# Kernel tuning notes

Measured on AMD Instinct MI355X. Metric: run time of the kernel, lower is better.

Reference implementation:

```python
import jax, jax.numpy as jnp
import numpy as np

B, T, H, L = 32, 512, 1024, 3


def setup_inputs() -> dict:
    key = jax.random.key(0)
    k1, k2, k3, k4 = jax.random.split(key, 4)
    scale = H ** -0.5  # stand-in for orthogonal init scale
    x = jax.random.normal(k1, (B, T, H), dtype=jnp.float32)
    h_0 = jax.random.normal(k2, (L, B, H), dtype=jnp.float32)
    w_ih = jax.random.normal(k3, (L, 3 * H, H), dtype=jnp.float32) * scale
    w_hh = jax.random.normal(k4, (L, 3 * H, H), dtype=jnp.float32) * scale
    b_ih = jnp.zeros((L, 3 * H), dtype=jnp.float32)  # module zero-inits biases
    b_hh = jnp.zeros((L, 3 * H), dtype=jnp.float32)
    return {"x": x, "h_0": h_0, "w_ih": w_ih, "w_hh": w_hh, "b_ih": b_ih, "b_hh": b_hh}


def _gru_layer(x_seq, h0, w_ih, w_hh, b_ih, b_hh):
    # Precompute input-side gate projections for all timesteps in one GEMM.
    gi = jnp.einsum('bti,gi->btg', x_seq, w_ih) + b_ih  # [B,T,3H]
    gi = jnp.transpose(gi, (1, 0, 2))  # [T,B,3H]

    def step(h, gi_t):
        gh = h @ w_hh.T + b_hh  # [B,3H]
        i_r, i_z, i_n = jnp.split(gi_t, 3, axis=-1)
        h_r, h_z, h_n = jnp.split(gh, 3, axis=-1)
        r = jax.nn.sigmoid(i_r + h_r)
        z = jax.nn.sigmoid(i_z + h_z)
        n = jnp.tanh(i_n + r * h_n)
        h_new = (1.0 - z) * n + z * h
        return h_new, h_new

    h_last, out = jax.lax.scan(step, h0, gi)  # out: [T,B,H]
    return jnp.transpose(out, (1, 0, 2)), h_last


def reference(x, h_0, w_ih, w_hh, b_ih, b_hh):
    # Multi-layer batch_first GRU, dropout=0 (inference-equivalent).
    h_n = []
    seq = x
    for l in range(L):
        seq, h_last = _gru_layer(seq, h_0[l], w_ih[l], w_hh[l], b_ih[l], b_hh[l])
        h_n.append(h_last)
    return seq, jnp.stack(h_n, axis=0)  # out:[B,T,H], h_n:[L,B,H]
```

## Files before the change

### kernel.cpp

```cpp
#include <hip/hip_runtime.h>
#include <hip/hip_bf16.h>
#include <stdint.h>

#define HD   1024
#define BB   32
#define TT   512
#define LL   3
#define H3   3072
#define MTOT (BB*TT)

#define PLSZ 32768
#define WSL2 12288

typedef unsigned short u16;
typedef short bf16x8 __attribute__((ext_vector_type(8)));
typedef float f32x4 __attribute__((ext_vector_type(4)));

__device__ __forceinline__ u16 f2bf_bits(float f) {
    __hip_bfloat16 h = __float2bfloat16(f);
    return __builtin_bit_cast(u16, h);
}
__device__ __forceinline__ float bf_bits2f(u16 b) {
    return __bfloat162float(__builtin_bit_cast(__hip_bfloat16, b));
}

__device__ __forceinline__ void split8(const f32x4 v0, const f32x4 v1,
                                       bf16x8& hi, bf16x8& lo) {
#pragma unroll
    for (int e = 0; e < 4; ++e) {
        u16 h = f2bf_bits(v0[e]);
        hi[e] = (short)h;
        lo[e] = (short)f2bf_bits(v0[e] - bf_bits2f(h));
        u16 h2 = f2bf_bits(v1[e]);
        hi[4 + e] = (short)h2;
        lo[4 + e] = (short)f2bf_bits(v1[e] - bf_bits2f(h2));
    }
}

__global__ void split_f32_kernel(const float* __restrict__ in,
                                 u16* __restrict__ hi, u16* __restrict__ lo, int n4) {
    int i = blockIdx.x * blockDim.x + threadIdx.x;
    int stride = gridDim.x * blockDim.x;
    for (; i < n4; i += stride) {
        float4 v = ((const float4*)in)[i];
        ushort4 h, l;
        float f;
        f = v.x; h.x = f2bf_bits(f); l.x = f2bf_bits(f - bf_bits2f(h.x));
        f = v.y; h.y = f2bf_bits(f); l.y = f2bf_bits(f - bf_bits2f(h.y));
        f = v.z; h.z = f2bf_bits(f); l.z = f2bf_bits(f - bf_bits2f(h.z));
        f = v.w; h.w = f2bf_bits(f); l.w = f2bf_bits(f - bf_bits2f(h.w));
        ((ushort4*)hi)[i] = h;
        ((ushort4*)lo)[i] = l;
    }
}

__global__ void tobf_kernel(const float* __restrict__ in, u16* __restrict__ out, int n4) {
    int i = blockIdx.x * blockDim.x + threadIdx.x;
    int stride = gridDim.x * blockDim.x;
    for (; i < n4; i += stride) {
        float4 v = ((const float4*)in)[i];
        ushort4 h;
        h.x = f2bf_bits(v.x); h.y = f2bf_bits(v.y);
        h.z = f2bf_bits(v.z); h.w = f2bf_bits(v.w);
        ((ushort4*)out)[i] = h;
    }
}

__global__ __launch_bounds__(256) void pack_w_kernel(
    const float* __restrict__ whh, const float* __restrict__ wih,
    u16* __restrict__ wslab, u16* __restrict__ wislab)
{
    const int l  = blockIdx.x >> 8;
    const int ug = blockIdx.x & 255;
    const int n0 = ug * 4;
    const int tid = threadIdx.x;
    const int j = tid >> 4, c16 = tid & 15;
    if (j >= 12) return;
    const size_t rowoff = ((size_t)(j >> 2) * HD + n0 + (j & 3)) * HD;
    const float* wh = whh + (size_t)l * H3 * HD;
    const float* wi = wih + (size_t)l * H3 * HD;
    u16* dh = wslab + ((size_t)l * 256 + ug) * WSL2;
    u16* di = (l > 0) ? (wislab + ((size_t)(l - 1) * 256 + ug) * WSL2) : (u16*)nullptr;
#pragma unroll
    for (int c = 0; c < 8; ++c) {
        int kc = c16 + c * 16;
        f32x4 v0 = *(const f32x4*)(wh + rowoff + kc * 8);
        f32x4 v1 = *(const f32x4*)(wh + rowoff + kc * 8 + 4);
        bf16x8 hi, lo;
        split8(v0, v1, hi, lo);
        *(bf16x8*)(dh + (kc * 12 + j) * 8) = hi;
        if (l > 0) {
            f32x4 u0 = *(const f32x4*)(wi + rowoff + kc * 8);
            f32x4 u1 = *(const f32x4*)(wi + rowoff + kc * 8 + 4);
            bf16x8 ihi, dum;
            split8(u0, u1, ihi, dum);
            *(bf16x8*)(di + (kc * 12 + j) * 8) = ihi;
        }
    }
}

__global__ void pack_h0_kernel(const float* __restrict__ h0,
                               float* __restrict__ hb, u16* __restrict__ ht) {
    int idx = blockIdx.x * 256 + threadIdx.x;
    int l = idx >> 15;
    int rem = idx & 32767;
    int b = rem >> 10, n = rem & 1023;
    float f = h0[idx];
    hb[(size_t)(l * 2) * BB * HD + rem] = f;
    u16 hbits = f2bf_bits(f);
    u16 lbits = f2bf_bits(f - bf_bits2f(hbits));
    size_t o = ((size_t)(l * 2) * 2) * PLSZ + ((size_t)(n >> 3) * 32 + b) * 8 + (n & 7);
    ht[o] = hbits;
    ht[o + PLSZ] = lbits;
}

#define BM 128
#define BN 128
#define BK 32
#define LDSROW 40

__global__ __launch_bounds__(256) void gemm2p_kernel(
    const u16* __restrict__ Ahi, const u16* __restrict__ Alo,
    const u16* __restrict__ Wn,
    const float* __restrict__ bias,
    u16* __restrict__ Cout)
{
    __shared__ u16 sAh[BM * LDSROW];
    __shared__ u16 sAl[BM * LDSROW];
    __shared__ u16 sB [BN * LDSROW];

    const int tid  = threadIdx.x;
    const int lane = tid & 63;
    const int w    = tid >> 6;
    const int wr   = w >> 1, wc = w & 1;
    const int fr   = lane & 15;
    const int kg   = lane >> 4;

    const int bm = blockIdx.x & 127;
    const int bn = blockIdx.x >> 7;
    const int bmBase = bm * BM;
    const int bnBase = bn * BN;

    f32x4 acc[4][4] = {};

    for (int kt = 0; kt < 1024; kt += BK) {
        uint4 ra[2], rl[2], rb[2];
#pragma unroll
        for (int it = 0; it < 2; ++it) {
            int c = it * 256 + tid;
            int row = c >> 2, seg = c & 3;
            size_t ga = (size_t)(bmBase + row) * 1024 + kt + seg * 8;
            ra[it] = *(const uint4*)(Ahi + ga);
            rl[it] = *(const uint4*)(Alo + ga);
            size_t gb = (size_t)(bnBase + row) * 1024 + kt + seg * 8;
            rb[it] = *(const uint4*)(Wn + gb);
        }
        __syncthreads();
#pragma unroll
        for (int it = 0; it < 2; ++it) {
            int c = it * 256 + tid;
            int row = c >> 2, seg = c & 3;
            int lo = row * LDSROW + seg * 8;
            *(uint4*)(sAh + lo) = ra[it];
            *(uint4*)(sAl + lo) = rl[it];
            *(uint4*)(sB  + lo) = rb[it];
        }
        __syncthreads();

        bf16x8 fah[4], fal[4], fb[4];
#pragma unroll
        for (int mi = 0; mi < 4; ++mi) {
            int r = wr * 64 + mi * 16 + fr;
            fah[mi] = *(const bf16x8*)(sAh + r * LDSROW + kg * 8);
            fal[mi] = *(const bf16x8*)(sAl + r * LDSROW + kg * 8);
        }
#pragma unroll
        for (int ni = 0; ni < 4; ++ni) {
            int r = wc * 64 + ni * 16 + fr;
            fb[ni] = *(const bf16x8*)(sB + r * LDSROW + kg * 8);
        }
#pragma unroll
        for (int mi = 0; mi < 4; ++mi)
#pragma unroll
            for (int ni = 0; ni < 4; ++ni) {
                acc[mi][ni] = __builtin_amdgcn_mfma_f32_16x16x32_bf16(fah[mi], fb[ni], acc[mi][ni], 0, 0, 0);
                acc[mi][ni] = __builtin_amdgcn_mfma_f32_16x16x32_bf16(fal[mi], fb[ni], acc[mi][ni], 0, 0, 0);
            }
    }

#pragma unroll
    for (int mi = 0; mi < 4; ++mi)
#pragma unroll
        for (int ni = 0; ni < 4; ++ni) {
            int n = bnBase + wc * 64 + ni * 16 + fr;
            float bv = bias[n];
#pragma unroll
            for (int r = 0; r < 4; ++r) {
                int m = bmBase + wr * 64 + mi * 16 + kg * 4 + r;
                int b_ = m >> 9, t_ = m & 511;
                Cout[(size_t)(t_ * BB + b_) * H3 + n] = f2bf_bits(acc[mi][ni][r] + bv);
            }
        }
}

#define SGRID 768

__global__ __launch_bounds__(256) void gru_step_kernel(
    const u16* __restrict__ wslab,
    const u16* __restrict__ wislab,
    const float* __restrict__ bih, const float* __restrict__ bhh,
    const u16* __restrict__ gi0,
    float* __restrict__ hb,
    u16* __restrict__ ht,
    float* __restrict__ seqout, float* __restrict__ hnout, int k)
{
    const int layer = blockIdx.x >> 8;
    const int t = k - layer;
    if (t < 0 || t >= TT) return;
    const int ug = blockIdx.x & 255;
    const int n0 = ug * 4;
    const int tid = threadIdx.x, lane = tid & 63, w = tid >> 6;
    const int arow = lane & 15, akg = lane >> 4;

    __shared__ float Cp[4][2][2][16][16];

    const int xl = (layer > 0) ? layer - 1 : 0;
    const u16* hsH = ht + ((size_t)(layer * 2 + (t & 1)) * 2) * PLSZ;
    const u16* hsL = hsH + PLSZ;
    const u16* xsH = ht + ((size_t)(xl * 2 + ((t + 1) & 1)) * 2) * PLSZ;
    const u16* xsL = xsH + PLSZ;
    const u16* whH = wslab + ((size_t)layer * 256 + ug) * WSL2;
    const u16* wiH = wislab + ((size_t)xl * 256 + ug) * WSL2;

    float gi_0 = 0.f, gi_1 = 0.f, gi_2 = 0.f;
    if (layer == 0 && tid < 128) {
        const u16* gp = gi0 + (size_t)(t * BB + (tid >> 2)) * H3 + n0 + (tid & 3);
        gi_0 = bf_bits2f(gp[0]);
        gi_1 = bf_bits2f(gp[HD]);
        gi_2 = bf_bits2f(gp[2 * HD]);
    }

    f32x4 agh[2] = {};
    f32x4 agx[2] = {};

#pragma unroll
    for (int kt = 0; kt < 8; ++kt) {
        const int kc = w * 32 + kt * 4 + akg;
        const int aoff = (kc * 32 + arow) * 8;
        bf16x8 a0h = *(const bf16x8*)(hsH + aoff);
        bf16x8 a0l = *(const bf16x8*)(hsL + aoff);
        bf16x8 a1h = *(const bf16x8*)(hsH + aoff + 128);
        bf16x8 a1l = *(const bf16x8*)(hsL + aoff + 128);
        bf16x8 bh = {}, bi = {};
        if (arow < 12) {
            bh = *(const bf16x8*)(whH + (kc * 12 + arow) * 8);
            if (layer > 0) bi = *(const bf16x8*)(wiH + (kc * 12 + arow) * 8);
        }
        agh[0] = __builtin_amdgcn_mfma_f32_16x16x32_bf16(a0h, bh, agh[0], 0, 0, 0);
        agh[0] = __builtin_amdgcn_mfma_f32_16x16x32_bf16(a0l, bh, agh[0], 0, 0, 0);
        agh[1] = __builtin_amdgcn_mfma_f32_16x16x32_bf16(a1h, bh, agh[1], 0, 0, 0);
        agh[1] = __builtin_amdgcn_mfma_f32_16x16x32_bf16(a1l, bh, agh[1], 0, 0, 0);
        if (layer > 0) {
            bf16x8 x0h = *(const bf16x8*)(xsH + aoff);
            bf16x8 x0l = *(const bf16x8*)(xsL + aoff);
            bf16x8 x1h = *(const bf16x8*)(xsH + aoff + 128);
            bf16x8 x1l = *(const bf16x8*)(xsL + aoff + 128);
            agx[0] = __builtin_amdgcn_mfma_f32_16x16x32_bf16(x0h, bi, agx[0], 0, 0, 0);
            agx[0] = __builtin_amdgcn_mfma_f32_16x16x32_bf16(x0l, bi, agx[0], 0, 0, 0);
            agx[1] = __builtin_amdgcn_mfma_f32_16x16x32_bf16(x1h, bi, agx[1], 0, 0, 0);
            agx[1] = __builtin_amdgcn_mfma_f32_16x16x32_bf16(x1l, bi, agx[1], 0, 0, 0);
        }
    }

#pragma unroll
    for (int m = 0; m < 2; ++m)
#pragma unroll
        for (int i = 0; i < 4; ++i)
            Cp[w][0][m][akg * 4 + i][arow] = agh[m][i];
    if (layer > 0) {
#pragma unroll
        for (int m = 0; m < 2; ++m)
#pragma unroll
            for (int i = 0; i < 4; ++i)
                Cp[w][1][m][akg * 4 + i][arow] = agx[m][i];
    }
    __syncthreads();

    if (tid < 128) {
        const int b = tid >> 2, u = tid & 3;
        const int m = b >> 4, r = b & 15;
        const int n = n0 + u;
        float gh0 = 0.f, gh1 = 0.f, gh2 = 0.f;
#pragma unroll
        for (int ww = 0; ww < 4; ++ww) {
            gh0 += Cp[ww][0][m][r][u];
            gh1 += Cp[ww][0][m][r][4 + u];
            gh2 += Cp[ww][0][m][r][8 + u];
        }
        if (layer > 0) {
            float q0 = 0.f, q1 = 0.f, q2 = 0.f;
#pragma unroll
            for (int ww = 0; ww < 4; ++ww) {
                q0 += Cp[ww][1][m][r][u];
                q1 += Cp[ww][1][m][r][4 + u];
                q2 += Cp[ww][1][m][r][8 + u];
            }
            gi_0 = q0 + bih[layer * H3 + n];
            gi_1 = q1 + bih[layer * H3 + HD + n];
            gi_2 = q2 + bih[layer * H3 + 2 * HD + n];
        }
        const float bh0 = bhh[layer * H3 + n];
        const float bh1 = bhh[layer * H3 + HD + n];
        const float bh2 = bhh[layer * H3 + 2 * HD + n];
        const float hp = hb[(size_t)(layer * 2 + (t & 1)) * BB * HD + (size_t)b * HD + n];
        float rg = 1.f / (1.f + expf(-(gi_0 + gh0 + bh0)));
        float zg = 1.f / (1.f + expf(-(gi_1 + gh1 + bh1)));
        float ng = tanhf(gi_2 + rg * (gh2 + bh2));
        float hnew = (1.f - zg) * ng + zg * hp;
        hb[(size_t)(layer * 2 + ((t + 1) & 1)) * BB * HD + (size_t)b * HD + n] = hnew;
        u16 hbits = f2bf_bits(hnew);
        u16 lbits = f2bf_bits(hnew - bf_bits2f(hbits));
        size_t o = ((size_t)(layer * 2 + ((t + 1) & 1)) * 2) * PLSZ
                 + ((size_t)(n >> 3) * 32 + b) * 8 + (n & 7);
        ht[o] = hbits;
        ht[o + PLSZ] = lbits;
        if (layer == 2) seqout[((size_t)b * TT + t) * HD + n] = hnew;
        if (t == TT - 1) hnout[(size_t)layer * BB * HD + (size_t)b * HD + n] = hnew;
    }
}

extern "C" void kernel_launch(void* const* d_in, const int* in_sizes, int n_in,
                              void* d_out, int out_size, void* d_ws, size_t ws_size,
                              hipStream_t stream) {
    const float* x   = (const float*)d_in[0];
    const float* h0  = (const float*)d_in[1];
    const float* wih = (const float*)d_in[2];
    const float* whh = (const float*)d_in[3];
    const float* bih = (const float*)d_in[4];
    const float* bhh = (const float*)d_in[5];
    float* out = (float*)d_out;

    char* ws = (char*)d_ws;
    size_t off = 0;
    auto alloc = [&](size_t bytes) -> void* {
        void* p = ws + off;
        off += (bytes + 255) & ~(size_t)255;
        return p;
    };
    u16* gi     = (u16*)alloc((size_t)MTOT * H3 * 2);
    u16* p0h    = (u16*)alloc((size_t)MTOT * HD * 2);
    u16* p0l    = (u16*)alloc((size_t)MTOT * HD * 2);
    u16* wihb   = (u16*)alloc((size_t)H3 * HD * 2);
    u16* wslab  = (u16*)alloc((size_t)3 * 256 * WSL2 * 2);
    u16* wislab = (u16*)alloc((size_t)2 * 256 * WSL2 * 2);
    float* hb   = (float*)alloc((size_t)LL * 2 * BB * HD * 4);
    u16* ht     = (u16*)alloc((size_t)LL * 2 * 2 * PLSZ * 2);

    split_f32_kernel<<<2048, 256, 0, stream>>>(x, p0h, p0l, MTOT * HD / 4);
    tobf_kernel<<<2048, 256, 0, stream>>>(wih, wihb, H3 * HD / 4);
    pack_w_kernel<<<768, 256, 0, stream>>>(whh, wih, wslab, wislab);
    pack_h0_kernel<<<384, 256, 0, stream>>>(h0, hb, ht);

    float* seqbase = out;
    float* hnbase  = out + (size_t)BB * TT * HD;

    gemm2p_kernel<<<dim3(128 * 24), 256, 0, stream>>>(p0h, p0l, wihb, bih, gi);

    for (int k = 0; k < TT + LL - 1; ++k)
        gru_step_kernel<<<SGRID, 256, 0, stream>>>(
            wslab, wislab, bih, bhh, gi, hb, ht, seqbase, hnbase, k);
}
```

Before: 7.639 ms.

## Widen per-block hidden tile to 16 units with 8 waves and LDS atomic reduction

```diff
diff --git a/kernel.cpp b/kernel.cpp
--- a/kernel.cpp
+++ b/kernel.cpp
@@ -10,7 +10,7 @@
 #define MTOT (BB*TT)
 
 #define PLSZ 32768
-#define WSL2 12288
+#define WSL3 49152
 
 typedef unsigned short u16;
 typedef short bf16x8 __attribute__((ext_vector_type(8)));
@@ -70,31 +70,35 @@
     const float* __restrict__ whh, const float* __restrict__ wih,
     u16* __restrict__ wslab, u16* __restrict__ wislab)
 {
-    const int l  = blockIdx.x >> 8;
-    const int ug = blockIdx.x & 255;
-    const int n0 = ug * 4;
+    const int l  = blockIdx.x >> 6;
+    const int ug = blockIdx.x & 63;
+    const int n0 = ug * 16;
     const int tid = threadIdx.x;
-    const int j = tid >> 4, c16 = tid & 15;
-    if (j >= 12) return;
-    const size_t rowoff = ((size_t)(j >> 2) * HD + n0 + (j & 3)) * HD;
+    const int jr = tid >> 4, c16 = tid & 15;
     const float* wh = whh + (size_t)l * H3 * HD;
     const float* wi = wih + (size_t)l * H3 * HD;
-    u16* dh = wslab + ((size_t)l * 256 + ug) * WSL2;
-    u16* di = (l > 0) ? (wislab + ((size_t)(l - 1) * 256 + ug) * WSL2) : (u16*)nullptr;
-#pragma unroll
-    for (int c = 0; c < 8; ++c) {
-        int kc = c16 + c * 16;
-        f32x4 v0 = *(const f32x4*)(wh + rowoff + kc * 8);
-        f32x4 v1 = *(const f32x4*)(wh + rowoff + kc * 8 + 4);
-        bf16x8 hi, lo;
-        split8(v0, v1, hi, lo);
-        *(bf16x8*)(dh + (kc * 12 + j) * 8) = hi;
-        if (l > 0) {
-            f32x4 u0 = *(const f32x4*)(wi + rowoff + kc * 8);
-            f32x4 u1 = *(const f32x4*)(wi + rowoff + kc * 8 + 4);
-            bf16x8 ihi, dum;
-            split8(u0, u1, ihi, dum);
-            *(bf16x8*)(di + (kc * 12 + j) * 8) = ihi;
+    u16* dh = wslab + ((size_t)l * 64 + ug) * WSL3;
+    u16* di = (l > 0) ? (wislab + ((size_t)(l - 1) * 64 + ug) * WSL3) : (u16*)nullptr;
+#pragma unroll
+    for (int jj = 0; jj < 3; ++jj) {
+        int j = jj * 16 + jr;
+        int gate = j >> 4, u = j & 15;
+        const size_t rowoff = ((size_t)gate * HD + n0 + u) * HD;
+#pragma unroll
+        for (int c = 0; c < 8; ++c) {
+            int kc = c16 + c * 16;
+            f32x4 v0 = *(const f32x4*)(wh + rowoff + kc * 8);
+            f32x4 v1 = *(const f32x4*)(wh + rowoff + kc * 8 + 4);
+            bf16x8 hi, lo;
+            split8(v0, v1, hi, lo);
+            *(bf16x8*)(dh + ((size_t)kc * 48 + j) * 8) = hi;
+            if (l > 0) {
+                f32x4 u0 = *(const f32x4*)(wi + rowoff + kc * 8);
+                f32x4 u1 = *(const f32x4*)(wi + rowoff + kc * 8 + 4);
+                bf16x8 ihi, dum;
+                split8(u0, u1, ihi, dum);
+                *(bf16x8*)(di + ((size_t)kc * 48 + j) * 8) = ihi;
+            }
         }
     }
 }
@@ -203,9 +207,9 @@
         }
 }
 
-#define SGRID 768
-
-__global__ __launch_bounds__(256) void gru_step_kernel(
+#define SGRID 192
+
+__global__ __launch_bounds__(512, 2) void gru_step_kernel(
     const u16* __restrict__ wslab,
     const u16* __restrict__ wislab,
     const float* __restrict__ bih, const float* __restrict__ bhh,
@@ -214,100 +218,106 @@
     u16* __restrict__ ht,
     float* __restrict__ seqout, float* __restrict__ hnout, int k)
 {
-    const int layer = blockIdx.x >> 8;
+    const int layer = blockIdx.x >> 6;
     const int t = k - layer;
     if (t < 0 || t >= TT) return;
-    const int ug = blockIdx.x & 255;
-    const int n0 = ug * 4;
+    const int ug = blockIdx.x & 63;
+    const int n0 = ug * 16;
     const int tid = threadIdx.x, lane = tid & 63, w = tid >> 6;
     const int arow = lane & 15, akg = lane >> 4;
 
-    __shared__ float Cp[4][2][2][16][16];
+    __shared__ float Cp[2][3][2][16][16];
+
+#pragma unroll
+    for (int z = 0; z < 6; ++z)
+        ((float*)Cp)[tid + z * 512] = 0.f;
 
     const int xl = (layer > 0) ? layer - 1 : 0;
     const u16* hsH = ht + ((size_t)(layer * 2 + (t & 1)) * 2) * PLSZ;
     const u16* hsL = hsH + PLSZ;
     const u16* xsH = ht + ((size_t)(xl * 2 + ((t + 1) & 1)) * 2) * PLSZ;
     const u16* xsL = xsH + PLSZ;
-    const u16* whH = wslab + ((size_t)layer * 256 + ug) * WSL2;
-    const u16* wiH = wislab + ((size_t)xl * 256 + ug) * WSL2;
+    const u16* whH = wslab + ((size_t)layer * 64 + ug) * WSL3;
+    const u16* wiH = wislab + ((size_t)xl * 64 + ug) * WSL3;
 
     float gi_0 = 0.f, gi_1 = 0.f, gi_2 = 0.f;
-    if (layer == 0 && tid < 128) {
-        const u16* gp = gi0 + (size_t)(t * BB + (tid >> 2)) * H3 + n0 + (tid & 3);
+    if (layer == 0) {
+        const u16* gp = gi0 + (size_t)(t * BB + (tid >> 4)) * H3 + n0 + (tid & 15);
         gi_0 = bf_bits2f(gp[0]);
         gi_1 = bf_bits2f(gp[HD]);
         gi_2 = bf_bits2f(gp[2 * HD]);
     }
-
-    f32x4 agh[2] = {};
-    f32x4 agx[2] = {};
-
-#pragma unroll
-    for (int kt = 0; kt < 8; ++kt) {
-        const int kc = w * 32 + kt * 4 + akg;
+    __syncthreads();
+
+    f32x4 agh[3][2] = {};
+    f32x4 agx[3][2] = {};
+
+#pragma unroll
+    for (int kt = 0; kt < 4; ++kt) {
+        const int kc = w * 16 + kt * 4 + akg;
         const int aoff = (kc * 32 + arow) * 8;
         bf16x8 a0h = *(const bf16x8*)(hsH + aoff);
         bf16x8 a0l = *(const bf16x8*)(hsL + aoff);
         bf16x8 a1h = *(const bf16x8*)(hsH + aoff + 128);
         bf16x8 a1l = *(const bf16x8*)(hsL + aoff + 128);
-        bf16x8 bh = {}, bi = {};
-        if (arow < 12) {
-            bh = *(const bf16x8*)(whH + (kc * 12 + arow) * 8);
-            if (layer > 0) bi = *(const bf16x8*)(wiH + (kc * 12 + arow) * 8);
-        }
-        agh[0] = __builtin_amdgcn_mfma_f32_16x16x32_bf16(a0h, bh, agh[0], 0, 0, 0);
-        agh[0] = __builtin_amdgcn_mfma_f32_16x16x32_bf16(a0l, bh, agh[0], 0, 0, 0);
-        agh[1] = __builtin_amdgcn_mfma_f32_16x16x32_bf16(a1h, bh, agh[1], 0, 0, 0);
-        agh[1] = __builtin_amdgcn_mfma_f32_16x16x32_bf16(a1l, bh, agh[1], 0, 0, 0);
+        bf16x8 bh[3], bi[3];
+#pragma unroll
+        for (int nt = 0; nt < 3; ++nt)
+            bh[nt] = *(const bf16x8*)(whH + ((size_t)kc * 48 + nt * 16 + arow) * 8);
+#pragma unroll
+        for (int nt = 0; nt < 3; ++nt) {
+            agh[nt][0] = __builtin_amdgcn_mfma_f32_16x16x32_bf16(a0h, bh[nt], agh[nt][0], 0, 0, 0);
+            agh[nt][0] = __builtin_amdgcn_mfma_f32_16x16x32_bf16(a0l, bh[nt], agh[nt][0], 0, 0, 0);
+            agh[nt][1] = __builtin_amdgcn_mfma_f32_16x16x32_bf16(a1h, bh[nt], agh[nt][1], 0, 0, 0);
+            agh[nt][1] = __builtin_amdgcn_mfma_f32_16x16x32_bf16(a1l, bh[nt], agh[nt][1], 0, 0, 0);
+        }
         if (layer > 0) {
             bf16x8 x0h = *(const bf16x8*)(xsH + aoff);
             bf16x8 x0l = *(const bf16x8*)(xsL + aoff);
             bf16x8 x1h = *(const bf16x8*)(xsH + aoff + 128);
             bf16x8 x1l = *(const bf16x8*)(xsL + aoff + 128);
-            agx[0] = __builtin_amdgcn_mfma_f32_16x16x32_bf16(x0h, bi, agx[0], 0, 0, 0);
-            agx[0] = __builtin_amdgcn_mfma_f32_16x16x32_bf16(x0l, bi, agx[0], 0, 0, 0);
-            agx[1] = __builtin_amdgcn_mfma_f32_16x16x32_bf16(x1h, bi, agx[1], 0, 0, 0);
-            agx[1] = __builtin_amdgcn_mfma_f32_16x16x32_bf16(x1l, bi, agx[1], 0, 0, 0);
-        }
-    }
-
-#pragma unroll
-    for (int m = 0; m < 2; ++m)
-#pragma unroll
-        for (int i = 0; i < 4; ++i)
-            Cp[w][0][m][akg * 4 + i][arow] = agh[m][i];
+#pragma unroll
+            for (int nt = 0; nt < 3; ++nt)
+                bi[nt] = *(const bf16x8*)(wiH + ((size_t)kc * 48 + nt * 16 + arow) * 8);
+#pragma unroll
+            for (int nt = 0; nt < 3; ++nt) {
+                agx[nt][0] = __builtin_amdgcn_mfma_f32_16x16x32_bf16(x0h, bi[nt], agx[nt][0], 0, 0, 0);
+                agx[nt][0] = __builtin_amdgcn_mfma_f32_16x16x32_bf16(x0l, bi[nt], agx[nt][0], 0, 0, 0);
+                agx[nt][1] = __builtin_amdgcn_mfma_f32_16x16x32_bf16(x1h, bi[nt], agx[nt][1], 0, 0, 0);
+                agx[nt][1] = __builtin_amdgcn_mfma_f32_16x16x32_bf16(x1l, bi[nt], agx[nt][1], 0, 0, 0);
+            }
+        }
+    }
+
+#pragma unroll
+    for (int nt = 0; nt < 3; ++nt)
+#pragma unroll
+        for (int m = 0; m < 2; ++m)
+#pragma unroll
+            for (int i = 0; i < 4; ++i)
+                atomicAdd(&Cp[0][nt][m][akg * 4 + i][arow], agh[nt][m][i]);
     if (layer > 0) {
 #pragma unroll
-        for (int m = 0; m < 2; ++m)
-#pragma unroll
-            for (int i = 0; i < 4; ++i)
-                Cp[w][1][m][akg * 4 + i][arow] = agx[m][i];
+        for (int nt = 0; nt < 3; ++nt)
+#pragma unroll
+            for (int m = 0; m < 2; ++m)
+#pragma unroll
+                for (int i = 0; i < 4; ++i)
+                    atomicAdd(&Cp[1][nt][m][akg * 4 + i][arow], agx[nt][m][i]);
     }
     __syncthreads();
 
-    if (tid < 128) {
-        const int b = tid >> 2, u = tid & 3;
+    {
+        const int b = tid >> 4, u = tid & 15;
         const int m = b >> 4, r = b & 15;
         const int n = n0 + u;
-        float gh0 = 0.f, gh1 = 0.f, gh2 = 0.f;
-#pragma unroll
-        for (int ww = 0; ww < 4; ++ww) {
-            gh0 += Cp[ww][0][m][r][u];
-            gh1 += Cp[ww][0][m][r][4 + u];
-            gh2 += Cp[ww][0][m][r][8 + u];
-        }
+        float gh0 = Cp[0][0][m][r][u];
+        float gh1 = Cp[0][1][m][r][u];
+        float gh2 = Cp[0][2][m][r][u];
         if (layer > 0) {
-            float q0 = 0.f, q1 = 0.f, q2 = 0.f;
-#pragma unroll
-            for (int ww = 0; ww < 4; ++ww) {
-                q0 += Cp[ww][1][m][r][u];
-                q1 += Cp[ww][1][m][r][4 + u];
-                q2 += Cp[ww][1][m][r][8 + u];
-            }
-            gi_0 = q0 + bih[layer * H3 + n];
-            gi_1 = q1 + bih[layer * H3 + HD + n];
-            gi_2 = q2 + bih[layer * H3 + 2 * HD + n];
+            gi_0 = Cp[1][0][m][r][u] + bih[layer * H3 + n];
+            gi_1 = Cp[1][1][m][r][u] + bih[layer * H3 + HD + n];
+            gi_2 = Cp[1][2][m][r][u] + bih[layer * H3 + 2 * HD + n];
         }
         const float bh0 = bhh[layer * H3 + n];
         const float bh1 = bhh[layer * H3 + HD + n];
@@ -351,14 +361,14 @@
     u16* p0h    = (u16*)alloc((size_t)MTOT * HD * 2);
     u16* p0l    = (u16*)alloc((size_t)MTOT * HD * 2);
     u16* wihb   = (u16*)alloc((size_t)H3 * HD * 2);
-    u16* wslab  = (u16*)alloc((size_t)3 * 256 * WSL2 * 2);
-    u16* wislab = (u16*)alloc((size_t)2 * 256 * WSL2 * 2);
+    u16* wslab  = (u16*)alloc((size_t)3 * 64 * WSL3 * 2);
+    u16* wislab = (u16*)alloc((size_t)2 * 64 * WSL3 * 2);
     float* hb   = (float*)alloc((size_t)LL * 2 * BB * HD * 4);
     u16* ht     = (u16*)alloc((size_t)LL * 2 * 2 * PLSZ * 2);
 
     split_f32_kernel<<<2048, 256, 0, stream>>>(x, p0h, p0l, MTOT * HD / 4);
     tobf_kernel<<<2048, 256, 0, stream>>>(wih, wihb, H3 * HD / 4);
-    pack_w_kernel<<<768, 256, 0, stream>>>(whh, wih, wslab, wislab);
+    pack_w_kernel<<<192, 256, 0, stream>>>(whh, wih, wslab, wislab);
     pack_h0_kernel<<<384, 256, 0, stream>>>(h0, hb, ht);
 
     float* seqbase = out;
@@ -367,6 +377,6 @@
     gemm2p_kernel<<<dim3(128 * 24), 256, 0, stream>>>(p0h, p0l, wihb, bih, gi);
 
     for (int k = 0; k < TT + LL - 1; ++k)
-        gru_step_kernel<<<SGRID, 256, 0, stream>>>(
+        gru_step_kernel<<<SGRID, 512, 0, stream>>>(
             wslab, wislab, bih, bhh, gi, hb, ht, seqbase, hnbase, k);
 }
```

Result: slower. 21.15 ms (+176.9%).
